# Kernel optimization log

Hardware: AMD Instinct MI355X
Metric: run time of the kernel (lower is better)

## Reference

```python
import jax, jax.numpy as jnp
import numpy as np

NEG_SLOPE = 0.01

def lrelu(x):
    return jax.nn.leaky_relu(x, NEG_SLOPE)

def lin(x, w, b):
    # torch Linear: x @ W.T + b, W shape (out, in)
    return x @ w.T + b

def meansum_pool(mask, x_local, *x_global):
    # masked sum + mean over points, concat with global/context vectors
    x_sum = (x_local * mask).sum(axis=1)                 # (b, d)
    x_mean = x_sum / mask.sum(axis=1)                    # (b, d) / (b, 1)
    return jnp.concatenate([x_mean, x_sum, *x_global], axis=1)


def setup_inputs() -> dict:
    key = jax.random.key(0)
    ks = jax.random.split(key, 16)
    B, N, DIN, DC, H, G, NB, DOUT = 16, 8192, 3, 16, 128, 10, 6, 3

    def w(k, shape, fan_in):
        return (jax.random.normal(k, shape, jnp.float32) / np.float32(np.sqrt(fan_in)))

    inp = {
        "x_local": jax.random.normal(ks[0], (B, N, DIN), jnp.float32),
        "context": jax.random.normal(ks[1], (B, DC), jnp.float32),
        "mask": (jax.random.uniform(ks[2], (B, N, 1)) < 0.9).astype(jnp.float32),
        # EPiC_Projection params (effective weight-normed weights)
        "proj_lw": w(ks[3], (H, DIN), DIN), "proj_lb": jnp.zeros((H,), jnp.float32),
        "proj_g0w": w(ks[4], (H, 2 * H + DC), 2 * H + DC), "proj_g0b": jnp.zeros((H,), jnp.float32),
        "proj_g1w": w(ks[5], (H, H), H), "proj_g1b": jnp.zeros((H,), jnp.float32),
        "proj_g2w": w(ks[6], (G, H), H), "proj_g2b": jnp.zeros((G,), jnp.float32),
        # stacked per-block EPiC_layer params
        "g1w": w(ks[7], (NB, H, 2 * H + G + DC), 2 * H + G + DC), "g1b": jnp.zeros((NB, H), jnp.float32),
        "g2w": w(ks[8], (NB, G, H), H), "g2b": jnp.zeros((NB, G), jnp.float32),
        "l1w": w(ks[9], (NB, H, H + G + DC), H + G + DC), "l1b": jnp.zeros((NB, H), jnp.float32),
        "l2w": w(ks[10], (NB, H, H), H), "l2b": jnp.zeros((NB, H), jnp.float32),
        # output head
        "outw": w(ks[11], (DOUT, H), H), "outb": jnp.zeros((DOUT,), jnp.float32),
    }
    return inp


def reference(x_local, context, mask,
              proj_lw, proj_lb, proj_g0w, proj_g0b, proj_g1w, proj_g1b, proj_g2w, proj_g2b,
              g1w, g1b, g2w, g2b, l1w, l1b, l2w, l2b, outw, outb):
    B, N, _ = x_local.shape
    # --- EPiC_Projection ---
    xl = lrelu(lin(x_local, proj_lw, proj_lb))           # (b, n, H)
    xg = meansum_pool(mask, xl, context)                 # (b, 2H + DC)
    xg = lrelu(lin(xg, proj_g0w, proj_g0b))
    xg = lrelu(lin(xg, proj_g1w, proj_g1b))
    xg = lrelu(lin(xg, proj_g2w, proj_g2b))              # (b, G)
    xl = xl * mask
    # --- EPiC layers (no skip: use_skip_connection=False -> +0) ---
    num_blocks = g1w.shape[0]
    for i in range(num_blocks):
        pooled = meansum_pool(mask, xl, xg, context)     # (b, 2H + G + DC)
        h_g = lrelu(lin(pooled, g1w[i], g1b[i]))
        xg = lrelu(lin(h_g, g2w[i], g2b[i]) + xg)        # residual global
        xg_b = jnp.broadcast_to(xg[:, None, :], (B, N, xg.shape[-1]))
        ctx_b = jnp.broadcast_to(context[:, None, :], (B, N, context.shape[-1]))
        cat = jnp.concatenate([xl, xg_b, ctx_b], axis=2)  # (b, n, H + G + DC)
        h_l = lrelu(lin(cat, l1w[i], l1b[i]))
        xl = lrelu(lin(h_l, l2w[i], l2b[i]) + xl) * mask  # residual local, masked
    h = lin(xl, outw, outb)                              # (b, n, 3)
    return h * mask
```

## Files before the change

kernel.cpp:

```cpp
#include <hip/hip_runtime.h>
#include <hip/hip_bf16.h>


typedef __attribute__((ext_vector_type(8))) short short8;
typedef __attribute__((ext_vector_type(4))) float f32x4;

#define B_ 16
#define N_ 8192
#define DC_ 16
#define H_ 128
#define G_ 10
#define NB_ 6
#define NEG_ 0.01f

__device__ __forceinline__ float lrelu(float x) { return x > 0.f ? x : NEG_ * x; }

__device__ __forceinline__ unsigned short f2bf(float x) {
  union { float f; unsigned u; } v; v.f = x;
  return (unsigned short)((v.u + 0x7fffu + ((v.u >> 16) & 1u)) >> 16);
}
__device__ __forceinline__ float bf2f(unsigned short u) {
  union { unsigned u; float f; } v; v.u = ((unsigned)u) << 16; return v.f;
}
__device__ __forceinline__ void split_bf(float x, unsigned short& h, unsigned short& l) {
  union { float f; unsigned u; } v; v.f = x;
  unsigned hu = v.u & 0xffff0000u;
  h = (unsigned short)(hu >> 16);
  union { unsigned u; float f; } hv; hv.u = hu;
  l = f2bf(x - hv.f);
}

__device__ __forceinline__ f32x4 mfma16(short8 a, short8 b, f32x4 c) {
  return __builtin_amdgcn_mfma_f32_16x16x32_bf16(a, b, c, 0, 0, 0);
}

__device__ __forceinline__ void make_frags(f32x4 v0, f32x4 v1, short8& bh, short8& bl) {
  unsigned short h, l;
#pragma unroll
  for (int j = 0; j < 4; ++j) {
    split_bf(v0[j], h, l);
    bh[j] = (short)h; bl[j] = (short)l;
  }
#pragma unroll
  for (int j = 0; j < 4; ++j) {
    split_bf(v1[j], h, l);
    bh[4 + j] = (short)h; bl[4 + j] = (short)l;
  }
}

__device__ __forceinline__ void async_cp16(const void* g, void* l) {
  __builtin_amdgcn_global_load_lds(
      (const __attribute__((address_space(1))) void*)g,
      (__attribute__((address_space(3))) void*)l, 16, 0, 0);
}

__device__ __forceinline__ void agent_store(float* p, float v) {
  __hip_atomic_store(p, v, __ATOMIC_RELAXED, __HIP_MEMORY_SCOPE_AGENT);
}
__device__ __forceinline__ float agent_load(const float* p) {
  return __hip_atomic_load(p, __ATOMIC_RELAXED, __HIP_MEMORY_SCOPE_AGENT);
}

template <int NS>
__device__ void epic_global_tail(
    int b, int tid, const float* __restrict__ pP, float cnt,
    const float* __restrict__ xg_cur, float* __restrict__ xg_next,
    const float* __restrict__ context,
    const float* __restrict__ g1w_n, const float* __restrict__ g1b_n,
    const float* __restrict__ g2w_n, const float* __restrict__ g2b_n,
    const float* __restrict__ l1w_n, const float* __restrict__ l1b_n,
    float* __restrict__ gbias_out, float* shx) {
  if (tid < 256) {
    const int f = tid & 127, kh = tid >> 7;
    const float* pr = pP + ((size_t)b * NS + kh * (NS / 2)) * 128 + f;
    float s = 0.f;
#pragma unroll 8
    for (int w = 0; w < NS / 2; ++w) s += agent_load(pr + w * 128);
    shx[tid] = s;
  }
  __syncthreads();
  if (tid < 128) {
    float s = shx[tid] + shx[tid + 128];
    shx[384 + tid] = s;
    shx[256 + tid] = s / cnt;
  }
  if (tid < G_) shx[512 + tid] = xg_cur[tid];
  if (tid >= 32 && tid < 32 + DC_) shx[522 + tid - 32] = context[b * DC_ + tid - 32];
  __syncthreads();
  if (tid < 256) {
    const int f = tid & 127, kh = tid >> 7;
    const float* wr = g1w_n + (size_t)f * 282 + kh * 142;
    const float* vp = shx + 256 + kh * 142;
    const int n2 = kh ? 70 : 71;
    float a = 0.f;
#pragma unroll 8
    for (int j = 0; j < n2; ++j) {
      float2 w2 = *(const float2*)(wr + 2 * j);
      a += w2.x * vp[2 * j] + w2.y * vp[2 * j + 1];
    }
    shx[tid] = a;
  }
  __syncthreads();
  if (tid < 128) shx[544 + tid] = lrelu(shx[tid] + shx[tid + 128] + g1b_n[tid]);
  __syncthreads();
  if (tid < G_) {
    const float* wr = g2w_n + tid * 128;
    float a = g2b_n[tid] + shx[512 + tid];
#pragma unroll 8
    for (int j = 0; j < 32; ++j) {
      float4 w4 = *(const float4*)(wr + 4 * j);
      a += w4.x * shx[544 + 4 * j] + w4.y * shx[544 + 4 * j + 1] +
           w4.z * shx[544 + 4 * j + 2] + w4.w * shx[544 + 4 * j + 3];
    }
    float v = lrelu(a);
    shx[672 + tid] = v;
    xg_next[tid] = v;
  }
  __syncthreads();
  if (tid < 128) {
    const float* wr = l1w_n + tid * 154;
    float a = l1b_n[tid];
#pragma unroll
    for (int j = 0; j < G_; ++j) a += wr[128 + j] * shx[672 + j];
#pragma unroll
    for (int j = 0; j < DC_; ++j) a += wr[138 + j] * shx[522 + j];
    gbias_out[tid] = a;
  }
}

__global__ __launch_bounds__(256) void prep_weights(
    const float* __restrict__ l1w, const float* __restrict__ l2w,
    unsigned short* __restrict__ w1h, unsigned short* __restrict__ w1l,
    unsigned short* __restrict__ w2h, unsigned short* __restrict__ w2l,
    unsigned int* __restrict__ counters) {
  int idx = blockIdx.x * 256 + threadIdx.x;
  const int total = NB_ * H_ * H_;
  if (idx < 112) counters[idx] = 0u;
  if (idx < total) {
    int i = idx / (H_ * H_), rem = idx % (H_ * H_);
    int F = rem / H_, k = rem % H_;
    int mt = F >> 4, r = F & 15, ks = k >> 5, c = k & 31;
    int off = i * 16384 + (mt * 4 + ks) * 512 + ((c >> 3) * 16 + r) * 8 + (c & 7);
    unsigned short h, l;
    split_bf(l1w[(i * H_ + F) * 154 + k], h, l);
    w1h[off] = h; w1l[off] = l;
    split_bf(l2w[(i * H_ + F) * H_ + k], h, l);
    w2h[off] = h; w2l[off] = l;
  }
}

__global__ __launch_bounds__(256, 2) void proj_local_kernel(
    const float* __restrict__ xloc, const float* __restrict__ maskp,
    const float* __restrict__ plw, const float* __restrict__ plb,
    float* __restrict__ xlf, float* __restrict__ pP,
    float* __restrict__ cntp, float* __restrict__ cnt_g,
    unsigned int* __restrict__ counters,
    const float* __restrict__ context,
    const float* __restrict__ g0w, const float* __restrict__ g0b,
    const float* __restrict__ g1pw, const float* __restrict__ g1pb,
    const float* __restrict__ g2pw, const float* __restrict__ g2pb,
    float* __restrict__ xg_g,
    const float* __restrict__ g1w0, const float* __restrict__ g1b0,
    const float* __restrict__ g2w0, const float* __restrict__ g2b0,
    const float* __restrict__ l1w0, const float* __restrict__ l1b0,
    float* __restrict__ gbias_g) {
  __shared__ float wq[H_][4];
  __shared__ float wsum[512];
  __shared__ float cw[4];
  __shared__ float shx[768];
  __shared__ int winflag;
  const int tid = threadIdx.x, bid = blockIdx.x;
  const int wv = tid >> 6, lane = tid & 63;
  const int q = lane >> 4, n16 = lane & 15;
  const int b = bid >> 6;
  if (tid < H_) {
    wq[tid][0] = plw[tid * 3 + 0];
    wq[tid][1] = plw[tid * 3 + 1];
    wq[tid][2] = plw[tid * 3 + 2];
    wq[tid][3] = plb[tid];
  }
  __syncthreads();
  const int t = bid * 4 + wv;
  const int p0 = t * 32;
  const int pa = p0 + n16, pb = p0 + 16 + n16;
  const float xa0 = xloc[pa * 3], xa1 = xloc[pa * 3 + 1], xa2 = xloc[pa * 3 + 2];
  const float xb0 = xloc[pb * 3], xb1 = xloc[pb * 3 + 1], xb2 = xloc[pb * 3 + 2];
  const float m0 = maskp[pa], m1 = maskp[pb];
  float* ga = xlf + (size_t)(2 * t) * 2048;
  float* gb = ga + 2048;
#pragma unroll
  for (int ms = 0; ms < 8; ++ms) {
    f32x4 v0, v1;
#pragma unroll
    for (int r = 0; r < 4; ++r) {
      const int F = ms * 16 + q * 4 + r;
      float4 w4 = *(const float4*)wq[F];
      v0[r] = lrelu(w4.x * xa0 + w4.y * xa1 + w4.z * xa2 + w4.w) * m0;
      v1[r] = lrelu(w4.x * xb0 + w4.y * xb1 + w4.z * xb2 + w4.w) * m1;
    }
    *(f32x4*)(ga + ms * 256 + (q * 16 + n16) * 4) = v0;
    *(f32x4*)(gb + ms * 256 + (q * 16 + n16) * 4) = v1;
    f32x4 s = v0 + v1;
#pragma unroll
    for (int r = 0; r < 4; ++r) {
      float sv = s[r];
      sv += __shfl_xor(sv, 1, 64);
      sv += __shfl_xor(sv, 2, 64);
      sv += __shfl_xor(sv, 4, 64);
      sv += __shfl_xor(sv, 8, 64);
      s[r] = sv;
    }
    if (n16 == 0) *(f32x4*)&wsum[wv * 128 + ms * 16 + q * 4] = s;
  }
  {
    float c = (q == 0) ? (m0 + m1) : 0.f;
    c += __shfl_xor(c, 1, 64);
    c += __shfl_xor(c, 2, 64);
    c += __shfl_xor(c, 4, 64);
    c += __shfl_xor(c, 8, 64);
    if (lane == 0) cw[wv] = c;
  }
  __syncthreads();
  if (tid < 128) {
    agent_store(&pP[(size_t)(2 * bid) * 128 + tid], wsum[tid] + wsum[128 + tid]);
    agent_store(&pP[(size_t)(2 * bid + 1) * 128 + tid], wsum[256 + tid] + wsum[384 + tid]);
  }
  if (tid == 0) agent_store(&cntp[bid], cw[0] + cw[1] + cw[2] + cw[3]);

  __syncthreads();
  if (tid == 0) winflag = (atomicAdd(&counters[b], 1u) == 63u) ? 1 : 0;
  __syncthreads();
  if (!winflag) return;
  if (tid < 64) shx[688 + tid] = agent_load(&cntp[b * 64 + tid]);
  __syncthreads();
  if (tid == 0) {
    float c = 0.f;
#pragma unroll
    for (int w = 0; w < 64; ++w) c += shx[688 + w];
    shx[752] = c;
    cnt_g[b] = c;
  }
  __syncthreads();
  const float cnt = shx[752];
  {
    const int f = tid & 127, kh = tid >> 7;
    const float* pr = pP + ((size_t)b * 128 + kh * 64) * 128 + f;
    float s = 0.f;
#pragma unroll 8
    for (int w = 0; w < 64; ++w) s += agent_load(pr + w * 128);
    shx[tid] = s;
  }
  __syncthreads();
  if (tid < 128) {
    float s = shx[tid] + shx[tid + 128];
    shx[384 + tid] = s;
    shx[256 + tid] = s / cnt;
  }
  if (tid < DC_) shx[512 + tid] = context[b * DC_ + tid];
  __syncthreads();
  {
    const int f = tid & 127, kh = tid >> 7;
    const float* wr = g0w + (size_t)f * 272 + kh * 136;
    const float* vp = shx + 256 + kh * 136;
    float a = 0.f;
#pragma unroll 8
    for (int j = 0; j < 34; ++j) {
      float4 w4 = *(const float4*)(wr + 4 * j);
      a += w4.x * vp[4 * j] + w4.y * vp[4 * j + 1] + w4.z * vp[4 * j + 2] + w4.w * vp[4 * j + 3];
    }
    __syncthreads();
    shx[tid] = a;
  }
  __syncthreads();
  if (tid < 128) shx[544 + tid] = lrelu(shx[tid] + shx[tid + 128] + g0b[tid]);
  __syncthreads();
  {
    const int f = tid & 127, kh = tid >> 7;
    const float* wr = g1pw + (size_t)f * 128 + kh * 64;
    const float* vp = shx + 544 + kh * 64;
    float a = 0.f;
#pragma unroll 8
    for (int j = 0; j < 16; ++j) {
      float4 w4 = *(const float4*)(wr + 4 * j);
      a += w4.x * vp[4 * j] + w4.y * vp[4 * j + 1] + w4.z * vp[4 * j + 2] + w4.w * vp[4 * j + 3];
    }
    __syncthreads();
    shx[tid] = a;
  }
  __syncthreads();
  if (tid < 128) shx[544 + tid] = lrelu(shx[tid] + shx[tid + 128] + g1pb[tid]);
  __syncthreads();
  if (tid < G_) {
    const float* wr = g2pw + tid * 128;
    float a = g2pb[tid];
#pragma unroll 8
    for (int j = 0; j < 32; ++j) {
      float4 w4 = *(const float4*)(wr + 4 * j);
      a += w4.x * shx[544 + 4 * j] + w4.y * shx[544 + 4 * j + 1] +
           w4.z * shx[544 + 4 * j + 2] + w4.w * shx[544 + 4 * j + 3];
    }
    xg_g[(0 * 16 + b) * 16 + tid] = lrelu(a);
  }
  __syncthreads();
  epic_global_tail<128>(b, tid, pP, cnt,
                        xg_g + (0 * 16 + b) * 16, xg_g + (1 * 16 + b) * 16, context,
                        g1w0, g1b0, g2w0, g2b0, l1w0, l1b0,
                        gbias_g + (size_t)(0 * 16 + b) * 128, shx);
}

template <bool LAST>
__global__ __launch_bounds__(512, 2) void epic_local_kernel(
    float* __restrict__ xlf, float* __restrict__ pP,
    const float* __restrict__ cnt_g, unsigned int* __restrict__ counters_blk,
    const float* __restrict__ gbias_in,
    const float* __restrict__ xg_tail_cur, float* __restrict__ xg_tail_next,
    float* __restrict__ gbias_tail_out,
    const float* __restrict__ context,
    const float* __restrict__ g1w_n, const float* __restrict__ g1b_n,
    const float* __restrict__ g2w_n, const float* __restrict__ g2b_n,
    const float* __restrict__ l1w_n, const float* __restrict__ l1b_n,
    const float* __restrict__ l2b,
    const unsigned short* __restrict__ w1h, const unsigned short* __restrict__ w1l,
    const unsigned short* __restrict__ w2h, const unsigned short* __restrict__ w2l,
    const float* __restrict__ maskp,
    const float* __restrict__ outw, const float* __restrict__ outb,
    float* __restrict__ outp) {
  __shared__ unsigned short wbuf[65536];
  __shared__ float tiles[8][576];
  __shared__ float shx[768];
  __shared__ float gbias_s[128];
  __shared__ float l2b_s[128];
  __shared__ float wsum[1024];
  __shared__ float outw_s[392];
  __shared__ int winflag;
  const int tid = threadIdx.x, bid = blockIdx.x;
  const int b = bid >> 5;
  const int wv = tid >> 6, lane = tid & 63;
  const int q = lane >> 4, n16 = lane & 15;

  {
    const unsigned short* src =
        (wv < 2) ? w1h : (wv < 4) ? w1l : (wv < 6) ? w2h : w2l;
    const char* s8 = (const char*)(src + (wv & 1) * 8192) + lane * 16;
    char* d8 = (char*)wbuf + wv * 16384;
#pragma unroll
    for (int j = 0; j < 16; ++j) async_cp16(s8 + j * 1024, d8 + j * 1024);
  }
  if (tid < 128) {
    gbias_s[tid] = gbias_in[b * 128 + tid];
    l2b_s[tid] = l2b[tid];
  }
  if (LAST) {
    if (tid < 384) outw_s[tid] = outw[tid];
    if (tid >= 384 && tid < 387) outw_s[tid] = outb[tid - 384];
  }

  const int g0i = bid * 16 + wv * 2;
  short8 xbh[2][4], xbl[2][4];
#pragma unroll
  for (int nt = 0; nt < 2; ++nt) {
    const float* base_nt = xlf + (size_t)(g0i + nt) * 2048;
#pragma unroll
    for (int ks = 0; ks < 4; ++ks) {
      const float* pb = base_nt + (2 * ks + (q >> 1)) * 256 + ((q & 1) * 32 + n16) * 4;
      f32x4 v0 = *(const f32x4*)pb;
      f32x4 v1 = *(const f32x4*)(pb + 64);
      make_frags(v0, v1, xbh[nt][ks], xbl[nt][ks]);
    }
  }
  __syncthreads();

  const unsigned short* w1h_l = wbuf;
  const unsigned short* w1l_l = wbuf + 16384;
  const unsigned short* w2h_l = wbuf + 32768;
  const unsigned short* w2l_l = wbuf + 49152;
  float* T = tiles[wv];
  const int lane16 = lane * 8;

  f32x4 acc2[2][8];
#pragma unroll
  for (int nt = 0; nt < 2; ++nt)
#pragma unroll
    for (int ms = 0; ms < 8; ++ms) acc2[nt][ms] = (f32x4){0.f, 0.f, 0.f, 0.f};

#pragma unroll
  for (int ko = 0; ko < 4; ++ko) {
    f32x4 acc[2][2];
#pragma unroll
    for (int nt = 0; nt < 2; ++nt)
#pragma unroll
      for (int msl = 0; msl < 2; ++msl) acc[nt][msl] = (f32x4){0.f, 0.f, 0.f, 0.f};
#pragma unroll
    for (int msl = 0; msl < 2; ++msl) {
      short8 a1h[4], a1l[4];
#pragma unroll
      for (int ks = 0; ks < 4; ++ks) {
        const int off = ((ko * 2 + msl) * 4 + ks) * 512 + lane16;
        a1h[ks] = *(const short8*)(w1h_l + off);
        a1l[ks] = *(const short8*)(w1l_l + off);
      }
#pragma unroll
      for (int ks = 0; ks < 4; ++ks)
#pragma unroll
        for (int nt = 0; nt < 2; ++nt) {
          acc[nt][msl] = mfma16(a1h[ks], xbh[nt][ks], acc[nt][msl]);
          acc[nt][msl] = mfma16(a1l[ks], xbh[nt][ks], acc[nt][msl]);
          acc[nt][msl] = mfma16(a1h[ks], xbl[nt][ks], acc[nt][msl]);
        }
    }
    short8 b2h[2], b2l[2];
#pragma unroll
    for (int nt = 0; nt < 2; ++nt) {
#pragma unroll
      for (int msl = 0; msl < 2; ++msl) {
        f32x4 gb4 = *(const f32x4*)&gbias_s[(ko * 2 + msl) * 16 + q * 4];
        f32x4 hv;
#pragma unroll
        for (int r = 0; r < 4; ++r) hv[r] = lrelu(acc[nt][msl][r] + gb4[r]);
        *(f32x4*)&T[n16 * 36 + msl * 16 + q * 4] = hv;
      }
      __builtin_amdgcn_wave_barrier();
      {
        f32x4 h0 = *(const f32x4*)&T[n16 * 36 + q * 8];
        f32x4 h1 = *(const f32x4*)&T[n16 * 36 + q * 8 + 4];
        make_frags(h0, h1, b2h[nt], b2l[nt]);
      }
      __builtin_amdgcn_wave_barrier();
    }
#pragma unroll
    for (int half = 0; half < 2; ++half) {
      short8 a2h[4], a2l[4];
#pragma unroll
      for (int mi = 0; mi < 4; ++mi) {
        const int off = ((half * 4 + mi) * 4 + ko) * 512 + lane16;
        a2h[mi] = *(const short8*)(w2h_l + off);
        a2l[mi] = *(const short8*)(w2l_l + off);
      }
#pragma unroll
      for (int mi = 0; mi < 4; ++mi)
#pragma unroll
        for (int nt = 0; nt < 2; ++nt) {
          acc2[nt][half * 4 + mi] = mfma16(a2h[mi], b2h[nt], acc2[nt][half * 4 + mi]);
          acc2[nt][half * 4 + mi] = mfma16(a2l[mi], b2h[nt], acc2[nt][half * 4 + mi]);
          acc2[nt][half * 4 + mi] = mfma16(a2h[mi], b2l[nt], acc2[nt][half * 4 + mi]);
        }
    }
  }

  float mk[2];
#pragma unroll
  for (int nt = 0; nt < 2; ++nt) mk[nt] = maskp[(g0i + nt) * 16 + n16];
  f32x4 vsum[8];
  float po[2][3];
  if (!LAST) {
#pragma unroll
    for (int ms = 0; ms < 8; ++ms) vsum[ms] = (f32x4){0.f, 0.f, 0.f, 0.f};
  } else {
#pragma unroll
    for (int nt = 0; nt < 2; ++nt) po[nt][0] = po[nt][1] = po[nt][2] = 0.f;
  }
#pragma unroll
  for (int nt = 0; nt < 2; ++nt) {
    float* base_nt = xlf + (size_t)(g0i + nt) * 2048;
#pragma unroll
    for (int ms = 0; ms < 8; ++ms) {
      f32x4 lb4 = *(const f32x4*)&l2b_s[ms * 16 + q * 4];
      float* xo = base_nt + ms * 256 + (q * 16 + n16) * 4;
      f32x4 old = *(const f32x4*)xo;
      f32x4 v;
#pragma unroll
      for (int r = 0; r < 4; ++r) v[r] = lrelu(acc2[nt][ms][r] + lb4[r] + old[r]) * mk[nt];
      if (!LAST) {
        *(f32x4*)xo = v;
        vsum[ms] += v;
      } else {
        f32x4 w0 = *(const f32x4*)&outw_s[0 * 128 + ms * 16 + q * 4];
        f32x4 w1 = *(const f32x4*)&outw_s[1 * 128 + ms * 16 + q * 4];
        f32x4 w2 = *(const f32x4*)&outw_s[2 * 128 + ms * 16 + q * 4];
#pragma unroll
        for (int r = 0; r < 4; ++r) {
          po[nt][0] += v[r] * w0[r];
          po[nt][1] += v[r] * w1[r];
          po[nt][2] += v[r] * w2[r];
        }
      }
    }
  }
  if (LAST) {
#pragma unroll
    for (int nt = 0; nt < 2; ++nt)
#pragma unroll
      for (int o = 0; o < 3; ++o) {
        float s = po[nt][o];
        s += __shfl_xor(s, 16, 64);
        s += __shfl_xor(s, 32, 64);
        po[nt][o] = s;
      }
    if (q == 0) {
#pragma unroll
      for (int nt = 0; nt < 2; ++nt) {
        const int p = (g0i + nt) * 16 + n16;
#pragma unroll
        for (int o = 0; o < 3; ++o)
          outp[(size_t)p * 3 + o] = (po[nt][o] + outw_s[384 + o]) * mk[nt];
      }
    }
    return;
  }
#pragma unroll
  for (int ms = 0; ms < 8; ++ms) {
    f32x4 sr;
#pragma unroll
    for (int r = 0; r < 4; ++r) {
      float s = vsum[ms][r];
      s += __shfl_xor(s, 1, 64);
      s += __shfl_xor(s, 2, 64);
      s += __shfl_xor(s, 4, 64);
      s += __shfl_xor(s, 8, 64);
      sr[r] = s;
    }
    if (n16 == 0) *(f32x4*)&wsum[wv * 128 + ms * 16 + q * 4] = sr;
  }
  __syncthreads();
  if (tid < 128) {
    float s = 0.f;
#pragma unroll
    for (int w = 0; w < 8; ++w) s += wsum[w * 128 + tid];
    agent_store(&pP[(size_t)bid * 128 + tid], s);
  }

  __syncthreads();
  if (tid == 0) winflag = (atomicAdd(&counters_blk[b], 1u) == 31u) ? 1 : 0;
  __syncthreads();
  if (!winflag) return;
  epic_global_tail<32>(b, tid, pP, cnt_g[b], xg_tail_cur + b * 16, xg_tail_next + b * 16,
                       context, g1w_n, g1b_n, g2w_n, g2b_n, l1w_n, l1b_n,
                       gbias_tail_out + (size_t)b * 128, shx);
}

extern "C" void kernel_launch(void* const* d_in, const int* in_sizes, int n_in,
                              void* d_out, int out_size, void* d_ws, size_t ws_size,
                              hipStream_t stream) {
  const float* x_local = (const float*)d_in[0];
  const float* context = (const float*)d_in[1];
  const float* mask = (const float*)d_in[2];
  const float* proj_lw = (const float*)d_in[3];
  const float* proj_lb = (const float*)d_in[4];
  const float* proj_g0w = (const float*)d_in[5];
  const float* proj_g0b = (const float*)d_in[6];
  const float* proj_g1w = (const float*)d_in[7];
  const float* proj_g1b = (const float*)d_in[8];
  const float* proj_g2w = (const float*)d_in[9];
  const float* proj_g2b = (const float*)d_in[10];
  const float* g1w = (const float*)d_in[11];
  const float* g1b = (const float*)d_in[12];
  const float* g2w = (const float*)d_in[13];
  const float* g2b = (const float*)d_in[14];
  const float* l1w = (const float*)d_in[15];
  const float* l1b = (const float*)d_in[16];
  const float* l2w = (const float*)d_in[17];
  const float* l2b = (const float*)d_in[18];
  const float* outw = (const float*)d_in[19];
  const float* outb = (const float*)d_in[20];
  float* out = (float*)d_out;

  char* ws = (char*)d_ws;
  float* xlf = (float*)ws;
  float* pP = (float*)(ws + 67108864);
  float* cntp = (float*)(ws + 68157440);
  float* cnt_g = (float*)(ws + 68161536);
  float* xg_g = (float*)(ws + 68161600);
  float* gbias_g = (float*)(ws + 68168768);
  unsigned int* counters = (unsigned int*)(ws + 68217920);
  unsigned short* w1h = (unsigned short*)(ws + 68218368);
  unsigned short* w1l = (unsigned short*)(ws + 68414976);
  unsigned short* w2h = (unsigned short*)(ws + 68611584);
  unsigned short* w2l = (unsigned short*)(ws + 68808192);

  prep_weights<<<384, 256, 0, stream>>>(l1w, l2w, w1h, w1l, w2h, w2l, counters);
  proj_local_kernel<<<1024, 256, 0, stream>>>(
      x_local, mask, proj_lw, proj_lb, xlf, pP, cntp, cnt_g, counters, context,
      proj_g0w, proj_g0b, proj_g1w, proj_g1b, proj_g2w, proj_g2b, xg_g,
      g1w, g1b, g2w, g2b, l1w, l1b, gbias_g);
  for (int i = 0; i < NB_; ++i) {
    const int j = i + 1;
    const float* g1w_n = g1w + (size_t)j * 128 * 282;
    const float* g1b_n = g1b + j * 128;
    const float* g2w_n = g2w + j * 10 * 128;
    const float* g2b_n = g2b + j * 10;
    const float* l1w_n = l1w + (size_t)j * 128 * 154;
    const float* l1b_n = l1b + j * 128;
    const unsigned short* w1h_i = w1h + i * 16384;
    const unsigned short* w1l_i = w1l + i * 16384;
    const unsigned short* w2h_i = w2h + i * 16384;
    const unsigned short* w2l_i = w2l + i * 16384;
    if (i == NB_ - 1) {
      epic_local_kernel<true><<<512, 512, 0, stream>>>(
          xlf, pP, cnt_g, counters + (i + 1) * 16, gbias_g + (size_t)(i * 16) * 128,
          nullptr, nullptr, nullptr, context,
          nullptr, nullptr, nullptr, nullptr, nullptr, nullptr,
          l2b + i * 128, w1h_i, w1l_i, w2h_i, w2l_i, mask, outw, outb, out);
    } else {
      epic_local_kernel<false><<<512, 512, 0, stream>>>(
          xlf, pP, cnt_g, counters + (i + 1) * 16, gbias_g + (size_t)(i * 16) * 128,
          xg_g + (i + 1) * 16 * 16, xg_g + (i + 2) * 16 * 16,
          gbias_g + (size_t)((i + 1) * 16) * 128, context,
          g1w_n, g1b_n, g2w_n, g2b_n, l1w_n, l1b_n,
          l2b + i * 128, w1h_i, w1l_i, w2h_i, w2l_i, mask, outw, outb, out);
    }
  }
}
```

Baseline: 469.2 us.

## Permute W1 rows so layer-1 MFMA output feeds layer-2 directly; one tile per wave

The prep kernel now writes the first local weight in a row-permuted fragment layout. With that order, the layer-1 MFMA accumulators already sit in the B-operand layout that layer 2 needs, so the per-wave LDS transpose tile and its wave barriers are removed. Each block now runs 16 waves (1024 threads), with one 16-point tile per wave instead of two. The ko loop is no longer unrolled, which cuts register pressure. The trade is fewer independent MFMA chains per wave and a possible change in occupancy, since each 1024-thread block still needs the 128KB weight buffer in LDS.

```diff
diff --git a/kernel.cpp b/kernel.cpp
--- a/kernel.cpp
+++ b/kernel.cpp
@@ -139,13 +139,17 @@
   if (idx < total) {
     int i = idx / (H_ * H_), rem = idx % (H_ * H_);
     int F = rem / H_, k = rem % H_;
-    int mt = F >> 4, r = F & 15, ks = k >> 5, c = k & 31;
-    int off = i * 16384 + (mt * 4 + ks) * 512 + ((c >> 3) * 16 + r) * 8 + (c & 7);
+    int ks = k >> 5, c = k & 31;
+    int mt2 = F >> 4, r2 = F & 15;
+    int mt1 = ((F >> 5) << 1) | ((F >> 2) & 1);
+    int r1 = (((F >> 3) & 3) << 2) | (F & 3);
+    int off1 = i * 16384 + (mt1 * 4 + ks) * 512 + ((c >> 3) * 16 + r1) * 8 + (c & 7);
+    int off2 = i * 16384 + (mt2 * 4 + ks) * 512 + ((c >> 3) * 16 + r2) * 8 + (c & 7);
     unsigned short h, l;
     split_bf(l1w[(i * H_ + F) * 154 + k], h, l);
-    w1h[off] = h; w1l[off] = l;
+    w1h[off1] = h; w1l[off1] = l;
     split_bf(l2w[(i * H_ + F) * H_ + k], h, l);
-    w2h[off] = h; w2l[off] = l;
+    w2h[off2] = h; w2l[off2] = l;
   }
 }
 
@@ -309,7 +313,7 @@
 }
 
 template <bool LAST>
-__global__ __launch_bounds__(512, 2) void epic_local_kernel(
+__global__ __launch_bounds__(1024) void epic_local_kernel(
     float* __restrict__ xlf, float* __restrict__ pP,
     const float* __restrict__ cnt_g, unsigned int* __restrict__ counters_blk,
     const float* __restrict__ gbias_in,
@@ -326,11 +330,10 @@
     const float* __restrict__ outw, const float* __restrict__ outb,
     float* __restrict__ outp) {
   __shared__ unsigned short wbuf[65536];
-  __shared__ float tiles[8][576];
   __shared__ float shx[768];
   __shared__ float gbias_s[128];
   __shared__ float l2b_s[128];
-  __shared__ float wsum[1024];
+  __shared__ float wsum[2048];
   __shared__ float outw_s[392];
   __shared__ int winflag;
   const int tid = threadIdx.x, bid = blockIdx.x;
@@ -340,11 +343,11 @@
 
   {
     const unsigned short* src =
-        (wv < 2) ? w1h : (wv < 4) ? w1l : (wv < 6) ? w2h : w2l;
-    const char* s8 = (const char*)(src + (wv & 1) * 8192) + lane * 16;
-    char* d8 = (char*)wbuf + wv * 16384;
-#pragma unroll
-    for (int j = 0; j < 16; ++j) async_cp16(s8 + j * 1024, d8 + j * 1024);
+        (wv < 4) ? w1h : (wv < 8) ? w1l : (wv < 12) ? w2h : w2l;
+    const char* s8 = (const char*)(src + (wv & 3) * 4096) + lane * 16;
+    char* d8 = (char*)wbuf + wv * 8192;
+#pragma unroll
+    for (int j = 0; j < 8; ++j) async_cp16(s8 + j * 1024, d8 + j * 1024);
   }
   if (tid < 128) {
     gbias_s[tid] = gbias_in[b * 128 + tid];
@@ -355,18 +358,15 @@
     if (tid >= 384 && tid < 387) outw_s[tid] = outb[tid - 384];
   }
 
-  const int g0i = bid * 16 + wv * 2;
-  short8 xbh[2][4], xbl[2][4];
-#pragma unroll
-  for (int nt = 0; nt < 2; ++nt) {
-    const float* base_nt = xlf + (size_t)(g0i + nt) * 2048;
-#pragma unroll
-    for (int ks = 0; ks < 4; ++ks) {
-      const float* pb = base_nt + (2 * ks + (q >> 1)) * 256 + ((q & 1) * 32 + n16) * 4;
-      f32x4 v0 = *(const f32x4*)pb;
-      f32x4 v1 = *(const f32x4*)(pb + 64);
-      make_frags(v0, v1, xbh[nt][ks], xbl[nt][ks]);
-    }
+  const int g = bid * 16 + wv;
+  const float* base_g = xlf + (size_t)g * 2048;
+  short8 xbh[4], xbl[4];
+#pragma unroll
+  for (int ks = 0; ks < 4; ++ks) {
+    const float* pb = base_g + (2 * ks + (q >> 1)) * 256 + ((q & 1) * 32 + n16) * 4;
+    f32x4 v0 = *(const f32x4*)pb;
+    f32x4 v1 = *(const f32x4*)(pb + 64);
+    make_frags(v0, v1, xbh[ks], xbl[ks]);
   }
   __syncthreads();
 
@@ -374,136 +374,112 @@
   const unsigned short* w1l_l = wbuf + 16384;
   const unsigned short* w2h_l = wbuf + 32768;
   const unsigned short* w2l_l = wbuf + 49152;
-  float* T = tiles[wv];
   const int lane16 = lane * 8;
 
-  f32x4 acc2[2][8];
-#pragma unroll
-  for (int nt = 0; nt < 2; ++nt)
-#pragma unroll
-    for (int ms = 0; ms < 8; ++ms) acc2[nt][ms] = (f32x4){0.f, 0.f, 0.f, 0.f};
-
-#pragma unroll
+  f32x4 acc2[8];
+#pragma unroll
+  for (int ms = 0; ms < 8; ++ms) acc2[ms] = (f32x4){0.f, 0.f, 0.f, 0.f};
+
+#pragma unroll 1
   for (int ko = 0; ko < 4; ++ko) {
-    f32x4 acc[2][2];
-#pragma unroll
-    for (int nt = 0; nt < 2; ++nt)
-#pragma unroll
-      for (int msl = 0; msl < 2; ++msl) acc[nt][msl] = (f32x4){0.f, 0.f, 0.f, 0.f};
-#pragma unroll
-    for (int msl = 0; msl < 2; ++msl) {
-      short8 a1h[4], a1l[4];
-#pragma unroll
-      for (int ks = 0; ks < 4; ++ks) {
-        const int off = ((ko * 2 + msl) * 4 + ks) * 512 + lane16;
-        a1h[ks] = *(const short8*)(w1h_l + off);
-        a1l[ks] = *(const short8*)(w1l_l + off);
+    f32x4 acc[2];
+    acc[0] = (f32x4){0.f, 0.f, 0.f, 0.f};
+    acc[1] = (f32x4){0.f, 0.f, 0.f, 0.f};
+#pragma unroll
+    for (int t = 0; t < 2; ++t) {
+#pragma unroll
+      for (int kc = 0; kc < 2; ++kc) {
+        short8 a1h[2], a1l[2];
+#pragma unroll
+        for (int u = 0; u < 2; ++u) {
+          const int off = ((ko * 2 + t) * 4 + kc * 2 + u) * 512 + lane16;
+          a1h[u] = *(const short8*)(w1h_l + off);
+          a1l[u] = *(const short8*)(w1l_l + off);
+        }
+#pragma unroll
+        for (int u = 0; u < 2; ++u) {
+          const int ks = kc * 2 + u;
+          acc[t] = mfma16(a1h[u], xbh[ks], acc[t]);
+          acc[t] = mfma16(a1l[u], xbh[ks], acc[t]);
+          acc[t] = mfma16(a1h[u], xbl[ks], acc[t]);
+        }
       }
-#pragma unroll
-      for (int ks = 0; ks < 4; ++ks)
-#pragma unroll
-        for (int nt = 0; nt < 2; ++nt) {
-          acc[nt][msl] = mfma16(a1h[ks], xbh[nt][ks], acc[nt][msl]);
-          acc[nt][msl] = mfma16(a1l[ks], xbh[nt][ks], acc[nt][msl]);
-          acc[nt][msl] = mfma16(a1h[ks], xbl[nt][ks], acc[nt][msl]);
-        }
-    }
-    short8 b2h[2], b2l[2];
-#pragma unroll
-    for (int nt = 0; nt < 2; ++nt) {
-#pragma unroll
-      for (int msl = 0; msl < 2; ++msl) {
-        f32x4 gb4 = *(const f32x4*)&gbias_s[(ko * 2 + msl) * 16 + q * 4];
-        f32x4 hv;
-#pragma unroll
-        for (int r = 0; r < 4; ++r) hv[r] = lrelu(acc[nt][msl][r] + gb4[r]);
-        *(f32x4*)&T[n16 * 36 + msl * 16 + q * 4] = hv;
+    }
+    f32x4 gb0 = *(const f32x4*)&gbias_s[ko * 32 + q * 8];
+    f32x4 gb1 = *(const f32x4*)&gbias_s[ko * 32 + q * 8 + 4];
+    f32x4 hv0, hv1;
+#pragma unroll
+    for (int r = 0; r < 4; ++r) {
+      hv0[r] = lrelu(acc[0][r] + gb0[r]);
+      hv1[r] = lrelu(acc[1][r] + gb1[r]);
+    }
+    short8 b2h, b2l;
+    make_frags(hv0, hv1, b2h, b2l);
+#pragma unroll
+    for (int mc = 0; mc < 4; ++mc) {
+      short8 a2h[2], a2l[2];
+#pragma unroll
+      for (int u = 0; u < 2; ++u) {
+        const int off = ((mc * 2 + u) * 4 + ko) * 512 + lane16;
+        a2h[u] = *(const short8*)(w2h_l + off);
+        a2l[u] = *(const short8*)(w2l_l + off);
       }
-      __builtin_amdgcn_wave_barrier();
-      {
-        f32x4 h0 = *(const f32x4*)&T[n16 * 36 + q * 8];
-        f32x4 h1 = *(const f32x4*)&T[n16 * 36 + q * 8 + 4];
-        make_frags(h0, h1, b2h[nt], b2l[nt]);
+#pragma unroll
+      for (int u = 0; u < 2; ++u) {
+        const int ms = mc * 2 + u;
+        acc2[ms] = mfma16(a2h[u], b2h, acc2[ms]);
+        acc2[ms] = mfma16(a2l[u], b2h, acc2[ms]);
+        acc2[ms] = mfma16(a2h[u], b2l, acc2[ms]);
       }
-      __builtin_amdgcn_wave_barrier();
-    }
-#pragma unroll
-    for (int half = 0; half < 2; ++half) {
-      short8 a2h[4], a2l[4];
-#pragma unroll
-      for (int mi = 0; mi < 4; ++mi) {
-        const int off = ((half * 4 + mi) * 4 + ko) * 512 + lane16;
-        a2h[mi] = *(const short8*)(w2h_l + off);
-        a2l[mi] = *(const short8*)(w2l_l + off);
-      }
-#pragma unroll
-      for (int mi = 0; mi < 4; ++mi)
-#pragma unroll
-        for (int nt = 0; nt < 2; ++nt) {
-          acc2[nt][half * 4 + mi] = mfma16(a2h[mi], b2h[nt], acc2[nt][half * 4 + mi]);
-          acc2[nt][half * 4 + mi] = mfma16(a2l[mi], b2h[nt], acc2[nt][half * 4 + mi]);
-          acc2[nt][half * 4 + mi] = mfma16(a2h[mi], b2l[nt], acc2[nt][half * 4 + mi]);
-        }
-    }
-  }
-
-  float mk[2];
-#pragma unroll
-  for (int nt = 0; nt < 2; ++nt) mk[nt] = maskp[(g0i + nt) * 16 + n16];
+    }
+  }
+
+  const float mk = maskp[g * 16 + n16];
   f32x4 vsum[8];
-  float po[2][3];
+  float po[3];
   if (!LAST) {
 #pragma unroll
     for (int ms = 0; ms < 8; ++ms) vsum[ms] = (f32x4){0.f, 0.f, 0.f, 0.f};
   } else {
-#pragma unroll
-    for (int nt = 0; nt < 2; ++nt) po[nt][0] = po[nt][1] = po[nt][2] = 0.f;
-  }
-#pragma unroll
-  for (int nt = 0; nt < 2; ++nt) {
-    float* base_nt = xlf + (size_t)(g0i + nt) * 2048;
-#pragma unroll
-    for (int ms = 0; ms < 8; ++ms) {
-      f32x4 lb4 = *(const f32x4*)&l2b_s[ms * 16 + q * 4];
-      float* xo = base_nt + ms * 256 + (q * 16 + n16) * 4;
-      f32x4 old = *(const f32x4*)xo;
-      f32x4 v;
-#pragma unroll
-      for (int r = 0; r < 4; ++r) v[r] = lrelu(acc2[nt][ms][r] + lb4[r] + old[r]) * mk[nt];
-      if (!LAST) {
-        *(f32x4*)xo = v;
-        vsum[ms] += v;
-      } else {
-        f32x4 w0 = *(const f32x4*)&outw_s[0 * 128 + ms * 16 + q * 4];
-        f32x4 w1 = *(const f32x4*)&outw_s[1 * 128 + ms * 16 + q * 4];
-        f32x4 w2 = *(const f32x4*)&outw_s[2 * 128 + ms * 16 + q * 4];
-#pragma unroll
-        for (int r = 0; r < 4; ++r) {
-          po[nt][0] += v[r] * w0[r];
-          po[nt][1] += v[r] * w1[r];
-          po[nt][2] += v[r] * w2[r];
-        }
+    po[0] = po[1] = po[2] = 0.f;
+  }
+  float* base_w = xlf + (size_t)g * 2048;
+#pragma unroll
+  for (int ms = 0; ms < 8; ++ms) {
+    f32x4 lb4 = *(const f32x4*)&l2b_s[ms * 16 + q * 4];
+    float* xo = base_w + ms * 256 + (q * 16 + n16) * 4;
+    f32x4 old = *(const f32x4*)xo;
+    f32x4 v;
+#pragma unroll
+    for (int r = 0; r < 4; ++r) v[r] = lrelu(acc2[ms][r] + lb4[r] + old[r]) * mk;
+    if (!LAST) {
+      *(f32x4*)xo = v;
+      vsum[ms] += v;
+    } else {
+      f32x4 w0 = *(const f32x4*)&outw_s[0 * 128 + ms * 16 + q * 4];
+      f32x4 w1 = *(const f32x4*)&outw_s[1 * 128 + ms * 16 + q * 4];
+      f32x4 w2 = *(const f32x4*)&outw_s[2 * 128 + ms * 16 + q * 4];
+#pragma unroll
+      for (int r = 0; r < 4; ++r) {
+        po[0] += v[r] * w0[r];
+        po[1] += v[r] * w1[r];
+        po[2] += v[r] * w2[r];
       }
     }
   }
   if (LAST) {
 #pragma unroll
-    for (int nt = 0; nt < 2; ++nt)
-#pragma unroll
-      for (int o = 0; o < 3; ++o) {
-        float s = po[nt][o];
-        s += __shfl_xor(s, 16, 64);
-        s += __shfl_xor(s, 32, 64);
-        po[nt][o] = s;
-      }
+    for (int o = 0; o < 3; ++o) {
+      float s = po[o];
+      s += __shfl_xor(s, 16, 64);
+      s += __shfl_xor(s, 32, 64);
+      po[o] = s;
+    }
     if (q == 0) {
-#pragma unroll
-      for (int nt = 0; nt < 2; ++nt) {
-        const int p = (g0i + nt) * 16 + n16;
-#pragma unroll
-        for (int o = 0; o < 3; ++o)
-          outp[(size_t)p * 3 + o] = (po[nt][o] + outw_s[384 + o]) * mk[nt];
-      }
+      const int p = g * 16 + n16;
+#pragma unroll
+      for (int o = 0; o < 3; ++o)
+        outp[(size_t)p * 3 + o] = (po[o] + outw_s[384 + o]) * mk;
     }
     return;
   }
@@ -525,7 +501,7 @@
   if (tid < 128) {
     float s = 0.f;
 #pragma unroll
-    for (int w = 0; w < 8; ++w) s += wsum[w * 128 + tid];
+    for (int w = 0; w < 16; ++w) s += wsum[w * 128 + tid];
     agent_store(&pP[(size_t)bid * 128 + tid], s);
   }
 
@@ -595,13 +571,13 @@
     const unsigned short* w2h_i = w2h + i * 16384;
     const unsigned short* w2l_i = w2l + i * 16384;
     if (i == NB_ - 1) {
-      epic_local_kernel<true><<<512, 512, 0, stream>>>(
+      epic_local_kernel<true><<<512, 1024, 0, stream>>>(
           xlf, pP, cnt_g, counters + (i + 1) * 16, gbias_g + (size_t)(i * 16) * 128,
           nullptr, nullptr, nullptr, context,
           nullptr, nullptr, nullptr, nullptr, nullptr, nullptr,
           l2b + i * 128, w1h_i, w1l_i, w2h_i, w2l_i, mask, outw, outb, out);
     } else {
-      epic_local_kernel<false><<<512, 512, 0, stream>>>(
+      epic_local_kernel<false><<<512, 1024, 0, stream>>>(
           xlf, pP, cnt_g, counters + (i + 1) * 16, gbias_g + (size_t)(i * 16) * 128,
           xg_g + (i + 1) * 16 * 16, xg_g + (i + 2) * 16 * 16,
           gbias_g + (size_t)((i + 1) * 16) * 128, context,
```

After: 492.3 us. 1.05x slower.
